# Optimization experiments

Measured on AMD Instinct MI355X. Metric: run time of the kernel, lower is better.

## Reference

```python
import jax, jax.numpy as jnp
import numpy as np

NEG_INF = -10000.0  # matches torch.full((1,K), -10000.)
B, T, K = 256, 2048, 64

def setup_inputs() -> dict:
    key = jax.random.key(0)
    k1, k2 = jax.random.split(key)
    start_tag, stop_tag = K - 2, K - 1
    feats = jax.random.normal(k1, (B, T, K), dtype=jnp.float32)
    transitions = jax.random.normal(k2, (K, K), dtype=jnp.float32)
    # transitions[START, :] = -1e4 ; transitions[:, STOP] = -1e4 (as in __init__)
    transitions = transitions.at[start_tag, :].set(NEG_INF).at[:, stop_tag].set(NEG_INF)
    return {"feats": feats, "transitions": transitions,
            "start_tag": start_tag, "stop_tag": stop_tag}

def reference(feats, transitions, start_tag, stop_tag):
    """Batched Viterbi decode (module.forward): returns (path_score [B], best_path [B,T])."""
    Bn, Tn, Kn = feats.shape
    init = jnp.full((Bn, Kn), NEG_INF, feats.dtype).at[:, start_tag].set(0.0)
    feats_t = jnp.swapaxes(feats, 0, 1)  # [T, B, K]

    def vstep(fv, feat_t):
        # scores[b, next, prev] = fv[b, prev] + transitions[next, prev]
        scores = fv[:, None, :] + transitions[None, :, :]
        bp = jnp.argmax(scores, axis=-1).astype(jnp.int32)        # [B, K]
        fv_new = jnp.max(scores, axis=-1) + feat_t                # [B, K]
        return fv_new, bp

    fv_last, bps = jax.lax.scan(vstep, init, feats_t)             # bps: [T, B, K]
    terminal = fv_last + transitions[stop_tag][None, :]           # [B, K]
    best_last = jnp.argmax(terminal, axis=-1).astype(jnp.int32)   # [B]
    path_score = jnp.take_along_axis(terminal, best_last[:, None].astype(jnp.int32), axis=1)[:, 0]

    bidx = jnp.arange(Bn)
    def backtrace(tag, bp_t):
        prev = bp_t[bidx, tag]
        return prev, tag
    # reverse scan emits best_path[t] = tag chosen at timestep t; final carry is START
    _, path = jax.lax.scan(backtrace, best_last, bps, reverse=True)  # [T, B]
    return path_score, jnp.swapaxes(path, 0, 1)  # ([B], [B, T])
```

## Files before the change

kernel.cpp:

```cpp
#include <hip/hip_runtime.h>
#include <stdint.h>

#define BB 256
#define TT 2048
#define KK 64
#define CHUNK 64
#define NCHUNK (TT / CHUNK)
#define WARM 32
#define NSEG 16
#define SEGLEN (TT / NSEG)

__device__ __forceinline__ unsigned umax3(unsigned a, unsigned b, unsigned c) {
    return max(max(a, b), c);
}

__global__ __launch_bounds__(64, 4)
void viterbi_fwd_reg(const float* __restrict__ feats,
                     const float* __restrict__ trans,
                     const int* __restrict__ start_tag_p,
                     const int* __restrict__ stop_tag_p,
                     float* __restrict__ out,
                     unsigned char* __restrict__ bp_ws)
{
    const int bid  = blockIdx.x;
    const int b    = bid >> 4;
    const int s    = bid & 15;
    const int t0   = s * SEGLEN - (s ? WARM : 0);
    const int warmN = s ? WARM : 0;
    const int L    = warmN + SEGLEN;
    const int lane = threadIdx.x;

    const int start_tag = *start_tag_p;
    const int stop_tag  = *stop_tag_p;

    const float* fb = feats + (size_t)b * TT * KK + (size_t)t0 * KK + lane;
    unsigned char* bpb = bp_ws + (size_t)b * TT * KK;

    int trk[64];
#pragma unroll
    for (int p = 0; p < 64; ++p) {
        const float tv = fmaxf(trans[lane * KK + p], -256.0f);
        trk[p] = (((int)rintf(tv * 2048.0f)) << 6) | (63 - p);
    }

    int fv = ((s || lane == start_tag) ? (2048 * 2048) : (512 * 2048)) << 6;

    float r0 = fb[0 * KK], r1 = fb[1 * KK], r2 = fb[2 * KK], r3 = fb[3 * KK];

    auto stepf = [&](float featval, bool st, int tau) {
        const int fvb = fv;
        unsigned acc[8];
#pragma unroll
        for (int q = 0; q < 8; ++q) acc[q] = 0u;
#pragma unroll
        for (int p = 0; p < 64; ++p) {
            const int sp = __builtin_amdgcn_readlane(fvb, p);
            const unsigned c = (unsigned)(sp + trk[p]);
            acc[p & 7] = max(acc[p & 7], c);
        }
        const unsigned K = umax3(umax3(acc[0], acc[1], acc[2]),
                                 umax3(acc[3], acc[4], acc[5]),
                                 max(acc[6], acc[7]));
        if (st)
            bpb[(size_t)(t0 + tau) * KK + lane] = (unsigned char)(63 - (K & 63u));
        const int fsh = ((int)rintf(featval * 2048.0f)) << 6;
        fv = (int)(K & 0xFFFFFFC0u) + fsh;
    };

    for (int tau = 0; tau < warmN; tau += 4) {
        float n0 = fb[(tau + 4) * KK]; stepf(r0, false, tau + 0); r0 = n0;
        float n1 = fb[(tau + 5) * KK]; stepf(r1, false, tau + 1); r1 = n1;
        float n2 = fb[(tau + 6) * KK]; stepf(r2, false, tau + 2); r2 = n2;
        float n3 = fb[(tau + 7) * KK]; stepf(r3, false, tau + 3); r3 = n3;
    }
    for (int tau = warmN; tau < L; tau += 4) {
        float n0 = fb[min(tau + 4, L - 1) * KK]; stepf(r0, true, tau + 0); r0 = n0;
        float n1 = fb[min(tau + 5, L - 1) * KK]; stepf(r1, true, tau + 1); r1 = n1;
        float n2 = fb[min(tau + 6, L - 1) * KK]; stepf(r2, true, tau + 2); r2 = n2;
        float n3 = fb[min(tau + 7, L - 1) * KK]; stepf(r3, true, tau + 3); r3 = n3;
    }

    if (s == NSEG - 1) {
        const float fvf = (float)(fv >> 6) * (1.0f / 2048.0f);
        float bv = fvf + trans[stop_tag * KK + lane];
        int bi = lane;
#pragma unroll
        for (int off = 1; off < 64; off <<= 1) {
            const float ov = __shfl_xor(bv, off);
            const int   oi = __shfl_xor(bi, off);
            const bool take = (ov > bv) || (ov == bv && oi < bi);
            bv = take ? ov : bv;
            bi = take ? oi : bi;
        }
        if (lane == 0) out[b] = (float)bi;
    }
}

__global__ __launch_bounds__(512)
void viterbi_bt_score(const float* __restrict__ feats,
                      const float* __restrict__ trans,
                      const int* __restrict__ start_tag_p,
                      const int* __restrict__ stop_tag_p,
                      float* __restrict__ out,
                      const unsigned char* __restrict__ bp_ws)
{
    const int b    = blockIdx.x;
    const int tid  = threadIdx.x;
    const int lane = tid & 63;
    const int w    = __builtin_amdgcn_readfirstlane(tid >> 6);

    __shared__ int cmap[NCHUNK][KK];
    __shared__ int be_lds[NCHUNK];
    __shared__ unsigned char path_lds[TT];
    __shared__ float red_lds[8];

    const unsigned char* bpb = bp_ws + (size_t)b * TT * KK;

    {
        const int c0 = w * 4;
        const unsigned char* q0 = bpb + (size_t)(c0 + 0) * CHUNK * KK + lane;
        const unsigned char* q1 = bpb + (size_t)(c0 + 1) * CHUNK * KK + lane;
        const unsigned char* q2 = bpb + (size_t)(c0 + 2) * CHUNK * KK + lane;
        const unsigned char* q3 = bpb + (size_t)(c0 + 3) * CHUNK * KK + lane;
        int M0 = lane, M1 = lane, M2 = lane, M3 = lane;
        int a0 = q0[0], a1 = q1[0], a2 = q2[0], a3 = q3[0];
        int b0 = q0[KK], b1 = q1[KK], b2 = q2[KK], b3 = q3[KK];
        for (int t = 0; t < CHUNK; t += 2) {
            int n0 = 0, n1 = 0, n2 = 0, n3 = 0, m0 = 0, m1 = 0, m2 = 0, m3 = 0;
            if (t + 2 < CHUNK) {
                n0 = q0[(t + 2) * KK]; n1 = q1[(t + 2) * KK];
                n2 = q2[(t + 2) * KK]; n3 = q3[(t + 2) * KK];
                m0 = q0[(t + 3) * KK]; m1 = q1[(t + 3) * KK];
                m2 = q2[(t + 3) * KK]; m3 = q3[(t + 3) * KK];
            }
            M0 = __shfl(M0, a0); M1 = __shfl(M1, a1);
            M2 = __shfl(M2, a2); M3 = __shfl(M3, a3);
            M0 = __shfl(M0, b0); M1 = __shfl(M1, b1);
            M2 = __shfl(M2, b2); M3 = __shfl(M3, b3);
            a0 = n0; a1 = n1; a2 = n2; a3 = n3;
            b0 = m0; b1 = m1; b2 = m2; b3 = m3;
        }
        cmap[c0 + 0][lane] = M0; cmap[c0 + 1][lane] = M1;
        cmap[c0 + 2][lane] = M2; cmap[c0 + 3][lane] = M3;
    }
    __syncthreads();

    if (tid == 0) {
        int x = (int)out[b];
        be_lds[NCHUNK - 1] = x;
        for (int c = NCHUNK - 1; c >= 1; --c) {
            x = cmap[c][x];
            be_lds[c - 1] = x;
        }
    }
    __syncthreads();

    if (tid < NCHUNK) {
        const int c = tid;
        int x = be_lds[c];
        float* po = out + BB + (size_t)b * TT;
        for (int t = (c + 1) * CHUNK - 1; t >= c * CHUNK; --t) {
            po[t] = (float)x;
            path_lds[t] = (unsigned char)x;
            x = (int)bpb[(size_t)t * KK + x];
        }
    }
    __syncthreads();

    const float* fbb = feats + (size_t)b * TT * KK;
    const int start_tag = *start_tag_p;
    const int stop_tag  = *stop_tag_p;
    float acc = 0.0f;
    for (int t = tid; t < TT; t += 512) {
        const int xt = path_lds[t];
        const int xp = (t > 0) ? (int)path_lds[t - 1] : start_tag;
        acc += fbb[(size_t)t * KK + xt] + trans[xt * KK + xp];
    }
    if (tid == 0) acc += trans[stop_tag * KK + (int)path_lds[TT - 1]];
#pragma unroll
    for (int off = 1; off < 64; off <<= 1) acc += __shfl_xor(acc, off);
    if (lane == 0) red_lds[w] = acc;
    __syncthreads();
    if (tid == 0) {
        float sc = 0.0f;
        for (int i = 0; i < 8; ++i) sc += red_lds[i];
        out[b] = sc;
    }
}

extern "C" void kernel_launch(void* const* d_in, const int* in_sizes, int n_in,
                              void* d_out, int out_size, void* d_ws, size_t ws_size,
                              hipStream_t stream) {
    const float* feats = (const float*)d_in[0];
    const float* trans = (const float*)d_in[1];
    const int* start_tag = (const int*)d_in[2];
    const int* stop_tag  = (const int*)d_in[3];
    float* out = (float*)d_out;
    unsigned char* bp = (unsigned char*)d_ws;

    viterbi_fwd_reg<<<BB * NSEG, 64, 0, stream>>>(feats, trans, start_tag, stop_tag, out, bp);
    viterbi_bt_score<<<BB, 512, 0, stream>>>(feats, trans, start_tag, stop_tag, out, bp);
}
```

Before: 232.5 us.

## Split Viterbi max over previous tags across two waves with LDS reduction

```diff
diff --git a/kernel.cpp b/kernel.cpp
--- a/kernel.cpp
+++ b/kernel.cpp
@@ -14,13 +14,17 @@
     return max(max(a, b), c);
 }
 
-__global__ __launch_bounds__(64, 4)
-void viterbi_fwd_reg(const float* __restrict__ feats,
-                     const float* __restrict__ trans,
-                     const int* __restrict__ start_tag_p,
-                     const int* __restrict__ stop_tag_p,
-                     float* __restrict__ out,
-                     unsigned char* __restrict__ bp_ws)
+__device__ __forceinline__ void lds_barrier() {
+    asm volatile("s_waitcnt lgkmcnt(0)\n\ts_barrier" ::: "memory");
+}
+
+__global__ __launch_bounds__(128, 8)
+void viterbi_fwd_pm(const float* __restrict__ feats,
+                    const float* __restrict__ trans,
+                    const int* __restrict__ start_tag_p,
+                    const int* __restrict__ stop_tag_p,
+                    float* __restrict__ out,
+                    unsigned char* __restrict__ bp_ws)
 {
     const int bid  = blockIdx.x;
     const int b    = bid >> 4;
@@ -28,59 +32,73 @@
     const int t0   = s * SEGLEN - (s ? WARM : 0);
     const int warmN = s ? WARM : 0;
     const int L    = warmN + SEGLEN;
-    const int lane = threadIdx.x;
+    const int tid  = threadIdx.x;
+    const int lane = tid & 63;
+    const int w    = __builtin_amdgcn_readfirstlane(tid >> 6);
+    const int pb   = w * 32;
 
     const int start_tag = *start_tag_p;
     const int stop_tag  = *stop_tag_p;
 
+    __shared__ int part[2][2][KK];
+
     const float* fb = feats + (size_t)b * TT * KK + (size_t)t0 * KK + lane;
     unsigned char* bpb = bp_ws + (size_t)b * TT * KK;
 
-    int trk[64];
-#pragma unroll
-    for (int p = 0; p < 64; ++p) {
-        const float tv = fmaxf(trans[lane * KK + p], -256.0f);
-        trk[p] = (((int)rintf(tv * 2048.0f)) << 6) | (63 - p);
+    int trk[32];
+#pragma unroll
+    for (int i = 0; i < 32; ++i) {
+        const float tv = fmaxf(trans[lane * KK + pb + i], -256.0f);
+        trk[i] = (((int)rintf(tv * 2048.0f)) << 6) | (63 - (pb + i));
+        asm volatile("" : "+v"(trk[i]));
     }
 
     int fv = ((s || lane == start_tag) ? (2048 * 2048) : (512 * 2048)) << 6;
 
     float r0 = fb[0 * KK], r1 = fb[1 * KK], r2 = fb[2 * KK], r3 = fb[3 * KK];
 
-    auto stepf = [&](float featval, bool st, int tau) {
+    auto stepf = [&](int tau, float featval, bool st) {
         const int fvb = fv;
-        unsigned acc[8];
-#pragma unroll
-        for (int q = 0; q < 8; ++q) acc[q] = 0u;
-#pragma unroll
-        for (int p = 0; p < 64; ++p) {
-            const int sp = __builtin_amdgcn_readlane(fvb, p);
-            const unsigned c = (unsigned)(sp + trk[p]);
-            acc[p & 7] = max(acc[p & 7], c);
-        }
-        const unsigned K = umax3(umax3(acc[0], acc[1], acc[2]),
-                                 umax3(acc[3], acc[4], acc[5]),
-                                 max(acc[6], acc[7]));
-        if (st)
+        unsigned a0 = 0u, a1 = 0u, a2 = 0u, a3 = 0u;
+#pragma unroll
+        for (int i = 0; i < 32; i += 2) {
+            const int spA = __builtin_amdgcn_readlane(fvb, pb + i);
+            const int spB = __builtin_amdgcn_readlane(fvb, pb + i + 1);
+            const unsigned cA = (unsigned)(spA + trk[i]);
+            const unsigned cB = (unsigned)(spB + trk[i + 1]);
+            switch ((i >> 1) & 3) {
+                case 0: a0 = umax3(a0, cA, cB); break;
+                case 1: a1 = umax3(a1, cA, cB); break;
+                case 2: a2 = umax3(a2, cA, cB); break;
+                case 3: a3 = umax3(a3, cA, cB); break;
+            }
+        }
+        const unsigned kl = umax3(max(a0, a1), a2, a3);
+
+        part[tau & 1][w][lane] = kl;
+        lds_barrier();
+        const unsigned K = max(kl, (unsigned)part[tau & 1][w ^ 1][lane]);
+
+        if (st && w == 0)
             bpb[(size_t)(t0 + tau) * KK + lane] = (unsigned char)(63 - (K & 63u));
-        const int fsh = ((int)rintf(featval * 2048.0f)) << 6;
-        fv = (int)(K & 0xFFFFFFC0u) + fsh;
+
+        fv = (int)(K & 0xFFFFFFC0u) + (((int)rintf(featval * 2048.0f)) << 6);
     };
 
     for (int tau = 0; tau < warmN; tau += 4) {
-        float n0 = fb[(tau + 4) * KK]; stepf(r0, false, tau + 0); r0 = n0;
-        float n1 = fb[(tau + 5) * KK]; stepf(r1, false, tau + 1); r1 = n1;
-        float n2 = fb[(tau + 6) * KK]; stepf(r2, false, tau + 2); r2 = n2;
-        float n3 = fb[(tau + 7) * KK]; stepf(r3, false, tau + 3); r3 = n3;
+        float n0 = fb[(tau + 4) * KK]; stepf(tau + 0, r0, false); r0 = n0;
+        float n1 = fb[(tau + 5) * KK]; stepf(tau + 1, r1, false); r1 = n1;
+        float n2 = fb[(tau + 6) * KK]; stepf(tau + 2, r2, false); r2 = n2;
+        float n3 = fb[(tau + 7) * KK]; stepf(tau + 3, r3, false); r3 = n3;
     }
     for (int tau = warmN; tau < L; tau += 4) {
-        float n0 = fb[min(tau + 4, L - 1) * KK]; stepf(r0, true, tau + 0); r0 = n0;
-        float n1 = fb[min(tau + 5, L - 1) * KK]; stepf(r1, true, tau + 1); r1 = n1;
-        float n2 = fb[min(tau + 6, L - 1) * KK]; stepf(r2, true, tau + 2); r2 = n2;
-        float n3 = fb[min(tau + 7, L - 1) * KK]; stepf(r3, true, tau + 3); r3 = n3;
-    }
-
-    if (s == NSEG - 1) {
+        float n0 = fb[min(tau + 4, L - 1) * KK]; stepf(tau + 0, r0, true); r0 = n0;
+        float n1 = fb[min(tau + 5, L - 1) * KK]; stepf(tau + 1, r1, true); r1 = n1;
+        float n2 = fb[min(tau + 6, L - 1) * KK]; stepf(tau + 2, r2, true); r2 = n2;
+        float n3 = fb[min(tau + 7, L - 1) * KK]; stepf(tau + 3, r3, true); r3 = n3;
+    }
+
+    if (s == NSEG - 1 && w == 0) {
         const float fvf = (float)(fv >> 6) * (1.0f / 2048.0f);
         float bv = fvf + trans[stop_tag * KK + lane];
         int bi = lane;
@@ -198,6 +216,6 @@
     float* out = (float*)d_out;
     unsigned char* bp = (unsigned char*)d_ws;
 
-    viterbi_fwd_reg<<<BB * NSEG, 64, 0, stream>>>(feats, trans, start_tag, stop_tag, out, bp);
+    viterbi_fwd_pm<<<BB * NSEG, 128, 0, stream>>>(feats, trans, start_tag, stop_tag, out, bp);
     viterbi_bt_score<<<BB, 512, 0, stream>>>(feats, trans, start_tag, stop_tag, out, bp);
 }
```

After: 343.3 us. 47.6% more time.
